# Kernel tuning notes

Hardware: AMD Instinct MI355X
Metric: run time of the kernel (lower is better)

## Reference

```python
import jax, jax.numpy as jnp
import numpy as np

MAX_WAVELENGTH = 10000.0
NUM_HEADS = 15
NUM_KV_HEADS = 5
HEAD_DIM = 64


def apply_rope(x, positions):
    """RoPE: x [B, L, H, D], positions [B, L] (int)."""
    d_half = x.shape[-1] // 2
    x = x.astype(jnp.float32)
    freq_exponents = (2.0 / x.shape[-1]) * jnp.arange(d_half, dtype=jnp.float32)
    timescale = MAX_WAVELENGTH ** freq_exponents  # [d_half]
    radians = positions[..., None].astype(jnp.float32) / timescale  # [B, L, d_half]
    radians = radians[..., None, :]  # [B, L, 1, d_half]
    sin, cos = jnp.sin(radians), jnp.cos(radians)
    x1, x2 = x[..., :d_half], x[..., d_half:]
    return jnp.concatenate([x1 * cos - x2 * sin, x2 * cos + x1 * sin], axis=-1)


def setup_inputs() -> dict:
    key = jax.random.key(0)
    k1, k2, k3, k4 = jax.random.split(key, 4)
    B, L = 2, 2048
    query_states = jax.random.normal(k1, (B, L, NUM_HEADS, HEAD_DIM), dtype=jnp.float32)
    key_states = jax.random.normal(k2, (B, L, NUM_KV_HEADS, HEAD_DIM), dtype=jnp.float32)
    value_states = jax.random.normal(k3, (B, L, NUM_KV_HEADS, HEAD_DIM), dtype=jnp.float32)
    positions = jnp.sort(jax.random.randint(k4, (B, L), 0, L, dtype=jnp.int32), axis=-1)
    # Causal (prefix-LM) boolean mask [B, L, L]
    attention_mask = jnp.broadcast_to(jnp.tril(jnp.ones((L, L), dtype=bool)), (B, L, L))
    return {
        "query_states": query_states,
        "key_states": key_states,
        "value_states": value_states,
        "positions": positions,
        "attention_mask": attention_mask,
    }


def reference(query_states, key_states, value_states, positions, attention_mask):
    B, L = query_states.shape[0], query_states.shape[1]
    groups = NUM_HEADS // NUM_KV_HEADS  # 3

    # RoPE on Q and K (eager, per original module)
    q = apply_rope(query_states, positions)  # [B, L, 15, 64] fp32
    k = apply_rope(key_states, positions)    # [B, L, 5, 64]  fp32

    # GQA expansion: [B, L, Kv, D] -> [B, L, Kv*groups, D]
    k = jnp.repeat(k, groups, axis=2)
    v = jnp.repeat(value_states, groups, axis=2).astype(jnp.float32)

    # Scores in fp32: [B, H, Lq, Lk]
    scores = jnp.einsum("bqhd,bkhd->bhqk", q, k) * (HEAD_DIM ** -0.5)
    big_neg = jnp.finfo(jnp.float32).min
    scores = jnp.where(attention_mask[:, None, :, :], scores, big_neg)
    probs = jax.nn.softmax(scores, axis=-1)

    out = jnp.einsum("bhqk,bkhd->bqhd", probs, v)  # [B, L, H, D]
    return out.reshape(B, L, NUM_HEADS * HEAD_DIM)  # [B, L, 960]
```

## Files before the change

kernel.cpp:

```cpp
#include <hip/hip_runtime.h>
#include <math.h>

#define NB 2
#define NL 2048
#define NHQ 15
#define NKV 5
#define HD 64
#define NT 32
#define GRP 3
#define PST 72
#define NWB 40
#define CST 68
#define CSLOT (32 * CST + 32)

typedef __attribute__((ext_vector_type(8))) short short8;
typedef __attribute__((ext_vector_type(4))) float floatx4;

#define ROPE_C 0.28782313662425575f
#define QSCALE 0.18033688011116016f

__device__ __forceinline__ ushort f2bf(float x) {
    unsigned u = __builtin_bit_cast(unsigned, x);
    u = (u + 0x7FFFu + ((u >> 16) & 1u)) >> 16;
    return (ushort)u;
}
__device__ __forceinline__ unsigned pk2(float a, float b) {
    unsigned ua = __builtin_bit_cast(unsigned, a) + 0x8000u;
    unsigned ub = __builtin_bit_cast(unsigned, b) + 0x8000u;
    return __builtin_amdgcn_perm(ub, ua, 0x07060302u);
}

union U8  { short8 v; ushort u[8]; };
union F8  { float4 f4[2]; float f[8]; };

__global__ __launch_bounds__(256)
void prep_kv(const float* __restrict__ K, const float* __restrict__ V,
             const int* __restrict__ pos, ushort* __restrict__ Kr,
             ushort* __restrict__ Vr) {
    __shared__ float Vs[64][65];
    const int bid = blockIdx.x, t = threadIdx.x;
    if (bid < NB * NKV * NT) {
        int b = bid / (NKV * NT), rem = bid % (NKV * NT);
        int h = rem / NT, k0 = (rem % NT) * 64;
        int j = t >> 2, c0 = t & 3;
        int row = k0 + j;
        const float* src = K + ((size_t)((b * NL + row) * NKV + h)) * HD;
        int db = c0 * 8;
        F8 x1, x2;
        x1.f4[0] = *(const float4*)&src[db];
        x1.f4[1] = *(const float4*)&src[db + 4];
        x2.f4[0] = *(const float4*)&src[db + 32];
        x2.f4[1] = *(const float4*)&src[db + 36];
        float ps = (float)pos[b * NL + row];
        U8 lo, hi;
#pragma unroll
        for (int i = 0; i < 8; ++i) {
            float inv = __expf((float)(db + i) * -ROPE_C);
            float sn, cs; __sincosf(ps * inv, &sn, &cs);
            lo.u[i] = f2bf(x1.f[i] * cs - x2.f[i] * sn);
            hi.u[i] = f2bf(x2.f[i] * cs + x1.f[i] * sn);
        }
        ushort* dst = Kr + (size_t)bid * 4096;
        *(short8*)&dst[(((j >> 4)) * 64 + c0 * 16 + (j & 15)) * 8]     = lo.v;
        *(short8*)&dst[((4 + (j >> 4)) * 64 + c0 * 16 + (j & 15)) * 8] = hi.v;
    } else {
        int vb = bid - NB * NKV * NT;
        int b = vb / (NKV * NT), rem = vb % (NKV * NT);
        int h = rem / NT, k0 = (rem % NT) * 64;
#pragma unroll
        for (int it = 0; it < 4; ++it) {
            int e = t + it * 256;
            int j = e >> 4, d4 = (e & 15) * 4;
            *(float4*)&Vs[j][d4] =
                *(const float4*)&V[((size_t)((b * NL + k0 + j) * NKV + h)) * HD + d4];
        }
        __syncthreads();
        ushort* dst = Vr + (size_t)vb * 4096;
#pragma unroll
        for (int it = 0; it < 2; ++it) {
            int o = t + it * 256;
            int d = o >> 3, c = o & 7, j0 = c * 8;
            U8 r;
#pragma unroll
            for (int k = 0; k < 8; ++k) r.u[k] = f2bf(Vs[j0 + k][d]);
            *(short8*)&dst[(((c >> 2) * 4 + (d >> 4)) * 64 + (c & 3) * 16 + (d & 15)) * 8] = r.v;
        }
    }
}

__device__ __forceinline__ void tile_step(
    int kb, bool diag, int r0, int l16, int quad, int lane,
    const ushort* Kt0, const ushort* Vt0,
    const short8 (&Qa)[2][2], floatx4 (&O)[2][4], float (&lsum)[2],
    ushort* PbW)
{
    const ushort* kt = Kt0 + (size_t)kb * 4096;
    short8 kc[8];
#pragma unroll
    for (int i = 0; i < 8; ++i)
        kc[i] = *(const short8*)&kt[((size_t)i * 64 + lane) * 8];

    floatx4 S[2][4];
#pragma unroll
    for (int rf = 0; rf < 2; ++rf)
#pragma unroll
        for (int c = 0; c < 4; ++c) S[rf][c] = (floatx4){0.f, 0.f, 0.f, 0.f};
#pragma unroll
    for (int s = 0; s < 2; ++s)
#pragma unroll
        for (int c = 0; c < 4; ++c) {
            short8 kfv = kc[s * 4 + c];
            S[0][c] = __builtin_amdgcn_mfma_f32_16x16x32_bf16(kfv, Qa[0][s], S[0][c], 0, 0, 0);
            S[1][c] = __builtin_amdgcn_mfma_f32_16x16x32_bf16(kfv, Qa[1][s], S[1][c], 0, 0, 0);
        }

    if (diag) {
#pragma unroll
        for (int rf = 0; rf < 2; ++rf) {
            int qrow = r0 + rf * 16 + l16;
            float acc = 0.f;
#pragma unroll
            for (int c = 0; c < 4; ++c) {
                float pv[4];
#pragma unroll
                for (int r = 0; r < 4; ++r) {
                    int key = kb * 64 + c * 16 + quad * 4 + r;
                    float sv = S[rf][c][r];
                    if (key > qrow) sv = -1e30f;
                    pv[r] = exp2f(sv);
                    acc += pv[r];
                }
                *(uint2*)&PbW[rf * 16 * PST + l16 * PST + c * 16 + quad * 4] =
                    make_uint2(pk2(pv[0], pv[1]), pk2(pv[2], pv[3]));
            }
            lsum[rf] += acc;
        }
    } else {
#pragma unroll
        for (int rf = 0; rf < 2; ++rf) {
            float acc = 0.f;
#pragma unroll
            for (int c = 0; c < 4; ++c) {
                float pv[4];
#pragma unroll
                for (int r = 0; r < 4; ++r) {
                    pv[r] = exp2f(S[rf][c][r]);
                    acc += pv[r];
                }
                *(uint2*)&PbW[rf * 16 * PST + l16 * PST + c * 16 + quad * 4] =
                    make_uint2(pk2(pv[0], pv[1]), pk2(pv[2], pv[3]));
            }
            lsum[rf] += acc;
        }
    }

    const ushort* vt = Vt0 + (size_t)kb * 4096;
    short8 vc[8];
#pragma unroll
    for (int i = 0; i < 8; ++i)
        vc[i] = *(const short8*)&vt[((size_t)i * 64 + lane) * 8];

#pragma unroll
    for (int s = 0; s < 2; ++s) {
        short8 pf0 = *(const short8*)&PbW[0 * 16 * PST + l16 * PST + s * 32 + quad * 8];
        short8 pf1 = *(const short8*)&PbW[1 * 16 * PST + l16 * PST + s * 32 + quad * 8];
#pragma unroll
        for (int d = 0; d < 4; ++d) {
            short8 vfv = vc[s * 4 + d];
            O[0][d] = __builtin_amdgcn_mfma_f32_16x16x32_bf16(vfv, pf0, O[0][d], 0, 0, 0);
            O[1][d] = __builtin_amdgcn_mfma_f32_16x16x32_bf16(vfv, pf1, O[1][d], 0, 0, 0);
        }
    }
}

__global__ __launch_bounds__(256, 3)
void attn_flash(const float* __restrict__ Q, const ushort* __restrict__ Kr,
                const ushort* __restrict__ Vr, const int* __restrict__ pos,
                float* __restrict__ out) {
    __shared__ __align__(16) unsigned char smem[3 * CSLOT * sizeof(float)];

    const int t = threadIdx.x;
    const int w = t >> 6, lane = t & 63;
    const int l16 = lane & 15, quad = lane >> 4;

    const int bid  = blockIdx.x;
    const int work = (bid & 7) * 150 + (bid >> 3);
    const int bh   = work / NWB;
    const int beta = work % NWB;
    const int b = bh / NHQ, h = bh % NHQ;
    const int kvh = h / GRP;

    int qi, leaderw, nch;
    if (beta < 16)      { qi = 48 + beta; leaderw = 0; nch = 4; }
    else if (beta < 32) {
        if (w < 3)      { qi = 32 + (beta - 16); leaderw = 0; nch = 3; }
        else            { qi = beta - 16;        leaderw = 3; nch = 1; }
    } else {
        int c = beta - 32;
        if (w < 2)      { qi = 16 + 2 * c; leaderw = 0; nch = 2; }
        else            { qi = 17 + 2 * c; leaderw = 2; nch = 2; }
    }
    const int ntw   = (qi >> 1) + 1;
    const int chunk = w - leaderw;
    const int kb0   = (ntw * chunk) / nch;
    const int kb1   = (ntw * (chunk + 1)) / nch;
    const int r0    = qi * 32;

    const ushort* Kt0 = Kr + (size_t)((b * NKV + kvh) * NT) * 4096;
    const ushort* Vt0 = Vr + (size_t)((b * NKV + kvh) * NT) * 4096;
    ushort* PbW = (ushort*)smem + w * 2 * 16 * PST;

    short8 Qa[2][2];
#pragma unroll
    for (int rf = 0; rf < 2; ++rf) {
        int row = r0 + rf * 16 + l16;
        const float* src = Q + ((size_t)((b * NL + row) * NHQ + h)) * HD;
        int db = quad * 8;
        F8 x1, x2;
        x1.f4[0] = *(const float4*)&src[db];
        x1.f4[1] = *(const float4*)&src[db + 4];
        x2.f4[0] = *(const float4*)&src[db + 32];
        x2.f4[1] = *(const float4*)&src[db + 36];
        float ps = (float)pos[b * NL + row];
        union { short8 v; unsigned u[4]; } lo, hi;
#pragma unroll
        for (int i = 0; i < 8; i += 2) {
            float inv0 = __expf((float)(db + i) * -ROPE_C);
            float inv1 = __expf((float)(db + i + 1) * -ROPE_C);
            float sn0, cs0, sn1, cs1;
            __sincosf(ps * inv0, &sn0, &cs0);
            __sincosf(ps * inv1, &sn1, &cs1);
            float lo0 = (x1.f[i] * cs0 - x2.f[i] * sn0) * QSCALE;
            float lo1 = (x1.f[i + 1] * cs1 - x2.f[i + 1] * sn1) * QSCALE;
            float hi0 = (x2.f[i] * cs0 + x1.f[i] * sn0) * QSCALE;
            float hi1 = (x2.f[i + 1] * cs1 + x1.f[i + 1] * sn1) * QSCALE;
            lo.u[i >> 1] = pk2(lo0, lo1);
            hi.u[i >> 1] = pk2(hi0, hi1);
        }
        Qa[rf][0] = lo.v;
        Qa[rf][1] = hi.v;
    }

    floatx4 O[2][4];
    float lsum[2] = {0.f, 0.f};
#pragma unroll
    for (int rf = 0; rf < 2; ++rf)
#pragma unroll
        for (int d = 0; d < 4; ++d) O[rf][d] = (floatx4){0.f, 0.f, 0.f, 0.f};

    for (int kb = kb0; kb < kb1; ++kb)
        tile_step(kb, kb == ntw - 1, r0, l16, quad, lane, Kt0, Vt0,
                  Qa, O, lsum, PbW);

    float ls[2];
#pragma unroll
    for (int rf = 0; rf < 2; ++rf) {
        float v = lsum[rf];
        v += __shfl_xor(v, 16, 64);
        v += __shfl_xor(v, 32, 64);
        ls[rf] = v;
    }

    __syncthreads();
    float* Cmb = (float*)smem;
    if (chunk > 0) {
        float* slot = Cmb + (size_t)(w - 1) * CSLOT;
#pragma unroll
        for (int rf = 0; rf < 2; ++rf) {
#pragma unroll
            for (int d = 0; d < 4; ++d) {
                *(float4*)&slot[(rf * 16 + l16) * CST + d * 16 + quad * 4] =
                    make_float4(O[rf][d][0], O[rf][d][1], O[rf][d][2], O[rf][d][3]);
            }
            if (quad == 0) slot[32 * CST + rf * 16 + l16] = ls[rf];
        }
    }
    __syncthreads();
    if (chunk == 0) {
        for (int m = 1; m < nch; ++m) {
            const float* slot = Cmb + (size_t)(w + m - 1) * CSLOT;
#pragma unroll
            for (int rf = 0; rf < 2; ++rf) {
#pragma unroll
                for (int d = 0; d < 4; ++d) {
                    float4 x = *(const float4*)&slot[(rf * 16 + l16) * CST + d * 16 + quad * 4];
                    O[rf][d][0] += x.x; O[rf][d][1] += x.y;
                    O[rf][d][2] += x.z; O[rf][d][3] += x.w;
                }
                ls[rf] += slot[32 * CST + rf * 16 + l16];
            }
        }
#pragma unroll
        for (int rf = 0; rf < 2; ++rf) {
            float rinv = 1.0f / ls[rf];
            int qrow = r0 + rf * 16 + l16;
            float* op = out + (size_t)(b * NL + qrow) * (NHQ * HD) + h * HD;
#pragma unroll
            for (int d = 0; d < 4; ++d) {
                float4 o = make_float4(O[rf][d][0] * rinv, O[rf][d][1] * rinv,
                                       O[rf][d][2] * rinv, O[rf][d][3] * rinv);
                *(float4*)&op[d * 16 + quad * 4] = o;
            }
        }
    }
}

extern "C" void kernel_launch(void* const* d_in, const int* in_sizes, int n_in,
                              void* d_out, int out_size, void* d_ws, size_t ws_size,
                              hipStream_t stream) {
    const float* Q   = (const float*)d_in[0];
    const float* K   = (const float*)d_in[1];
    const float* V   = (const float*)d_in[2];
    const int*   pos = (const int*)d_in[3];
    ushort* Kr = (ushort*)d_ws;
    ushort* Vr = Kr + (size_t)NB * NKV * NT * 4096;
    float*  out = (float*)d_out;

    prep_kv<<<2 * NB * NKV * NT, 256, 0, stream>>>(K, V, pos, Kr, Vr);
    attn_flash<<<NB * NHQ * NWB, 256, 0, stream>>>(Q, Kr, Vr, pos, out);
}
```

Baseline: 137.2 us.

## Keep softmax probabilities in registers and use 16x16x16 MFMA for PV

Removes the per-wave LDS staging of the probability tile by packing exp values directly into bf16 short4 operands that match the 16x16x16 MFMA B-operand layout. The V tile prep is reorganized into the matching per-lane 4-element fragment layout, and the diagonal/non-diagonal branches are merged. This eliminates LDS stores/loads and their latency inside the loop, at the cost of twice as many smaller PV MFMA instructions and more V fragment registers.

```diff
diff --git a/kernel.cpp b/kernel.cpp
--- a/kernel.cpp
+++ b/kernel.cpp
@@ -8,12 +8,12 @@
 #define HD 64
 #define NT 32
 #define GRP 3
-#define PST 72
 #define NWB 40
 #define CST 68
 #define CSLOT (32 * CST + 32)
 
 typedef __attribute__((ext_vector_type(8))) short short8;
+typedef __attribute__((ext_vector_type(4))) short short4v;
 typedef __attribute__((ext_vector_type(4))) float floatx4;
 
 #define ROPE_C 0.28782313662425575f
@@ -30,8 +30,18 @@
     return __builtin_amdgcn_perm(ub, ua, 0x07060302u);
 }
 
+__device__ __forceinline__ floatx4 mfma16(short4v a, short4v b, floatx4 c) {
+#if __has_builtin(__builtin_amdgcn_mfma_f32_16x16x16bf16_1k)
+    return __builtin_amdgcn_mfma_f32_16x16x16bf16_1k(a, b, c, 0, 0, 0);
+#else
+    asm("v_mfma_f32_16x16x16_bf16 %0, %1, %2, %0" : "+v"(c) : "v"(a), "v"(b));
+    return c;
+#endif
+}
+
 union U8  { short8 v; ushort u[8]; };
 union F8  { float4 f4[2]; float f[8]; };
+union PU  { uint2 u2; short4v v; };
 
 __global__ __launch_bounds__(256)
 void prep_kv(const float* __restrict__ K, const float* __restrict__ V,
@@ -77,13 +87,18 @@
         __syncthreads();
         ushort* dst = Vr + (size_t)vb * 4096;
 #pragma unroll
-        for (int it = 0; it < 2; ++it) {
+        for (int it = 0; it < 4; ++it) {
             int o = t + it * 256;
-            int d = o >> 3, c = o & 7, j0 = c * 8;
-            U8 r;
-#pragma unroll
-            for (int k = 0; k < 8; ++k) r.u[k] = f2bf(Vs[j0 + k][d]);
-            *(short8*)&dst[(((c >> 2) * 4 + (d >> 4)) * 64 + (c & 3) * 16 + (d & 15)) * 8] = r.v;
+            int fi = o >> 6, lane = o & 63;
+            int d = fi >> 2, c = fi & 3;
+            int l16 = lane & 15, q = lane >> 4;
+            ushort a0 = f2bf(Vs[c * 16 + q * 4 + 0][d * 16 + l16]);
+            ushort a1 = f2bf(Vs[c * 16 + q * 4 + 1][d * 16 + l16]);
+            ushort a2 = f2bf(Vs[c * 16 + q * 4 + 2][d * 16 + l16]);
+            ushort a3 = f2bf(Vs[c * 16 + q * 4 + 3][d * 16 + l16]);
+            *(uint2*)&dst[(size_t)o * 4] =
+                make_uint2((unsigned)a0 | ((unsigned)a1 << 16),
+                           (unsigned)a2 | ((unsigned)a3 << 16));
         }
     }
 }
@@ -91,8 +106,7 @@
 __device__ __forceinline__ void tile_step(
     int kb, bool diag, int r0, int l16, int quad, int lane,
     const ushort* Kt0, const ushort* Vt0,
-    const short8 (&Qa)[2][2], floatx4 (&O)[2][4], float (&lsum)[2],
-    ushort* PbW)
+    const short8 (&Qa)[2][2], floatx4 (&O)[2][4], float (&lsum)[2])
 {
     const ushort* kt = Kt0 + (size_t)kb * 4096;
     short8 kc[8];
@@ -114,61 +128,44 @@
             S[1][c] = __builtin_amdgcn_mfma_f32_16x16x32_bf16(kfv, Qa[1][s], S[1][c], 0, 0, 0);
         }
 
-    if (diag) {
-#pragma unroll
-        for (int rf = 0; rf < 2; ++rf) {
-            int qrow = r0 + rf * 16 + l16;
-            float acc = 0.f;
-#pragma unroll
-            for (int c = 0; c < 4; ++c) {
-                float pv[4];
-#pragma unroll
-                for (int r = 0; r < 4; ++r) {
+    const ushort* vt = Vt0 + (size_t)kb * 4096;
+    short4v vc[16];
+#pragma unroll
+    for (int fi = 0; fi < 16; ++fi)
+        vc[fi] = *(const short4v*)&vt[((size_t)fi * 64 + lane) * 4];
+
+    short4v P[2][4];
+#pragma unroll
+    for (int rf = 0; rf < 2; ++rf) {
+        int qrow = r0 + rf * 16 + l16;
+        float acc = 0.f;
+#pragma unroll
+        for (int c = 0; c < 4; ++c) {
+            float pv[4];
+#pragma unroll
+            for (int r = 0; r < 4; ++r) {
+                float sv = S[rf][c][r];
+                if (diag) {
                     int key = kb * 64 + c * 16 + quad * 4 + r;
-                    float sv = S[rf][c][r];
                     if (key > qrow) sv = -1e30f;
-                    pv[r] = exp2f(sv);
-                    acc += pv[r];
                 }
-                *(uint2*)&PbW[rf * 16 * PST + l16 * PST + c * 16 + quad * 4] =
-                    make_uint2(pk2(pv[0], pv[1]), pk2(pv[2], pv[3]));
+                pv[r] = exp2f(sv);
+                acc += pv[r];
             }
-            lsum[rf] += acc;
-        }
-    } else {
-#pragma unroll
-        for (int rf = 0; rf < 2; ++rf) {
-            float acc = 0.f;
-#pragma unroll
-            for (int c = 0; c < 4; ++c) {
-                float pv[4];
-#pragma unroll
-                for (int r = 0; r < 4; ++r) {
-                    pv[r] = exp2f(S[rf][c][r]);
-                    acc += pv[r];
-                }
-                *(uint2*)&PbW[rf * 16 * PST + l16 * PST + c * 16 + quad * 4] =
-                    make_uint2(pk2(pv[0], pv[1]), pk2(pv[2], pv[3]));
-            }
-            lsum[rf] += acc;
-        }
-    }
-
-    const ushort* vt = Vt0 + (size_t)kb * 4096;
-    short8 vc[8];
-#pragma unroll
-    for (int i = 0; i < 8; ++i)
-        vc[i] = *(const short8*)&vt[((size_t)i * 64 + lane) * 8];
-
-#pragma unroll
-    for (int s = 0; s < 2; ++s) {
-        short8 pf0 = *(const short8*)&PbW[0 * 16 * PST + l16 * PST + s * 32 + quad * 8];
-        short8 pf1 = *(const short8*)&PbW[1 * 16 * PST + l16 * PST + s * 32 + quad * 8];
+            PU pu;
+            pu.u2 = make_uint2(pk2(pv[0], pv[1]), pk2(pv[2], pv[3]));
+            P[rf][c] = pu.v;
+        }
+        lsum[rf] += acc;
+    }
+
+#pragma unroll
+    for (int c = 0; c < 4; ++c) {
 #pragma unroll
         for (int d = 0; d < 4; ++d) {
-            short8 vfv = vc[s * 4 + d];
-            O[0][d] = __builtin_amdgcn_mfma_f32_16x16x32_bf16(vfv, pf0, O[0][d], 0, 0, 0);
-            O[1][d] = __builtin_amdgcn_mfma_f32_16x16x32_bf16(vfv, pf1, O[1][d], 0, 0, 0);
+            short4v vf = vc[d * 4 + c];
+            O[0][d] = mfma16(vf, P[0][c], O[0][d]);
+            O[1][d] = mfma16(vf, P[1][c], O[1][d]);
         }
     }
 }
@@ -177,7 +174,7 @@
 void attn_flash(const float* __restrict__ Q, const ushort* __restrict__ Kr,
                 const ushort* __restrict__ Vr, const int* __restrict__ pos,
                 float* __restrict__ out) {
-    __shared__ __align__(16) unsigned char smem[3 * CSLOT * sizeof(float)];
+    __shared__ __align__(16) float Cmb[3 * CSLOT];
 
     const int t = threadIdx.x;
     const int w = t >> 6, lane = t & 63;
@@ -208,7 +205,6 @@
 
     const ushort* Kt0 = Kr + (size_t)((b * NKV + kvh) * NT) * 4096;
     const ushort* Vt0 = Vr + (size_t)((b * NKV + kvh) * NT) * 4096;
-    ushort* PbW = (ushort*)smem + w * 2 * 16 * PST;
 
     short8 Qa[2][2];
 #pragma unroll
@@ -250,7 +246,7 @@
 
     for (int kb = kb0; kb < kb1; ++kb)
         tile_step(kb, kb == ntw - 1, r0, l16, quad, lane, Kt0, Vt0,
-                  Qa, O, lsum, PbW);
+                  Qa, O, lsum);
 
     float ls[2];
 #pragma unroll
@@ -262,7 +258,6 @@
     }
 
     __syncthreads();
-    float* Cmb = (float*)smem;
     if (chunk > 0) {
         float* slot = Cmb + (size_t)(w - 1) * CSLOT;
 #pragma unroll
```

New measurement: 147.0 us. +7.2%, slower.

## Precompute RoPE tables in prep kernel, hoist V loads, template diagonal tile

Applied to the files above, without the earlier changes.

The K-prep kernel now writes per-position cos/sin tables to workspace, and the attention kernel reads them for Q RoPE instead of computing exp/sincos itself. The software bf16 packing is replaced with the hardware v_cvt_pk_bf16_f32 instruction. V tile loads are issued together with K loads before the QK MFMAs, and the diagonal/masked tile is split out through a template so the main loop has no mask branch. These trade extra workspace traffic and higher register pressure for less transcendental math and earlier memory latency hiding.

```diff
diff --git a/kernel.cpp b/kernel.cpp
--- a/kernel.cpp
+++ b/kernel.cpp
@@ -24,10 +24,10 @@
     u = (u + 0x7FFFu + ((u >> 16) & 1u)) >> 16;
     return (ushort)u;
 }
-__device__ __forceinline__ unsigned pk2(float a, float b) {
-    unsigned ua = __builtin_bit_cast(unsigned, a) + 0x8000u;
-    unsigned ub = __builtin_bit_cast(unsigned, b) + 0x8000u;
-    return __builtin_amdgcn_perm(ub, ua, 0x07060302u);
+__device__ __forceinline__ unsigned cvtpk(float a, float b) {
+    unsigned r;
+    asm("v_cvt_pk_bf16_f32 %0, %1, %2" : "=v"(r) : "v"(a), "v"(b));
+    return r;
 }
 
 union U8  { short8 v; ushort u[8]; };
@@ -36,7 +36,8 @@
 __global__ __launch_bounds__(256)
 void prep_kv(const float* __restrict__ K, const float* __restrict__ V,
              const int* __restrict__ pos, ushort* __restrict__ Kr,
-             ushort* __restrict__ Vr) {
+             ushort* __restrict__ Vr, float* __restrict__ Tc,
+             float* __restrict__ Ts) {
     __shared__ float Vs[64][65];
     const int bid = blockIdx.x, t = threadIdx.x;
     if (bid < NB * NKV * NT) {
@@ -52,17 +53,26 @@
         x2.f4[0] = *(const float4*)&src[db + 32];
         x2.f4[1] = *(const float4*)&src[db + 36];
         float ps = (float)pos[b * NL + row];
-        U8 lo, hi;
+        U8 lo, hi; F8 snv, csv;
 #pragma unroll
         for (int i = 0; i < 8; ++i) {
             float inv = __expf((float)(db + i) * -ROPE_C);
             float sn, cs; __sincosf(ps * inv, &sn, &cs);
+            snv.f[i] = sn; csv.f[i] = cs;
             lo.u[i] = f2bf(x1.f[i] * cs - x2.f[i] * sn);
             hi.u[i] = f2bf(x2.f[i] * cs + x1.f[i] * sn);
         }
         ushort* dst = Kr + (size_t)bid * 4096;
         *(short8*)&dst[(((j >> 4)) * 64 + c0 * 16 + (j & 15)) * 8]     = lo.v;
         *(short8*)&dst[((4 + (j >> 4)) * 64 + c0 * 16 + (j & 15)) * 8] = hi.v;
+        if (rem < NT) {
+            float* tcp = Tc + ((size_t)(b * NL + row)) * 32 + db;
+            float* tsp = Ts + ((size_t)(b * NL + row)) * 32 + db;
+            *(float4*)&tcp[0] = csv.f4[0];
+            *(float4*)&tcp[4] = csv.f4[1];
+            *(float4*)&tsp[0] = snv.f4[0];
+            *(float4*)&tsp[4] = snv.f4[1];
+        }
     } else {
         int vb = bid - NB * NKV * NT;
         int b = vb / (NKV * NT), rem = vb % (NKV * NT);
@@ -88,17 +98,22 @@
     }
 }
 
+template<bool DIAG>
 __device__ __forceinline__ void tile_step(
-    int kb, bool diag, int r0, int l16, int quad, int lane,
+    int kb, int r0, int l16, int quad, int lane,
     const ushort* Kt0, const ushort* Vt0,
     const short8 (&Qa)[2][2], floatx4 (&O)[2][4], float (&lsum)[2],
     ushort* PbW)
 {
     const ushort* kt = Kt0 + (size_t)kb * 4096;
-    short8 kc[8];
+    const ushort* vt = Vt0 + (size_t)kb * 4096;
+    short8 kc[8], vc[8];
 #pragma unroll
     for (int i = 0; i < 8; ++i)
         kc[i] = *(const short8*)&kt[((size_t)i * 64 + lane) * 8];
+#pragma unroll
+    for (int i = 0; i < 8; ++i)
+        vc[i] = *(const short8*)&vt[((size_t)i * 64 + lane) * 8];
 
     floatx4 S[2][4];
 #pragma unroll
@@ -114,51 +129,28 @@
             S[1][c] = __builtin_amdgcn_mfma_f32_16x16x32_bf16(kfv, Qa[1][s], S[1][c], 0, 0, 0);
         }
 
-    if (diag) {
-#pragma unroll
-        for (int rf = 0; rf < 2; ++rf) {
-            int qrow = r0 + rf * 16 + l16;
-            float acc = 0.f;
-#pragma unroll
-            for (int c = 0; c < 4; ++c) {
-                float pv[4];
-#pragma unroll
-                for (int r = 0; r < 4; ++r) {
+#pragma unroll
+    for (int rf = 0; rf < 2; ++rf) {
+        int qrow = r0 + rf * 16 + l16;
+        float acc = 0.f;
+#pragma unroll
+        for (int c = 0; c < 4; ++c) {
+            float pv[4];
+#pragma unroll
+            for (int r = 0; r < 4; ++r) {
+                float sv = S[rf][c][r];
+                if (DIAG) {
                     int key = kb * 64 + c * 16 + quad * 4 + r;
-                    float sv = S[rf][c][r];
                     if (key > qrow) sv = -1e30f;
-                    pv[r] = exp2f(sv);
-                    acc += pv[r];
                 }
-                *(uint2*)&PbW[rf * 16 * PST + l16 * PST + c * 16 + quad * 4] =
-                    make_uint2(pk2(pv[0], pv[1]), pk2(pv[2], pv[3]));
+                pv[r] = exp2f(sv);
+                acc += pv[r];
             }
-            lsum[rf] += acc;
-        }
-    } else {
-#pragma unroll
-        for (int rf = 0; rf < 2; ++rf) {
-            float acc = 0.f;
-#pragma unroll
-            for (int c = 0; c < 4; ++c) {
-                float pv[4];
-#pragma unroll
-                for (int r = 0; r < 4; ++r) {
-                    pv[r] = exp2f(S[rf][c][r]);
-                    acc += pv[r];
-                }
-                *(uint2*)&PbW[rf * 16 * PST + l16 * PST + c * 16 + quad * 4] =
-                    make_uint2(pk2(pv[0], pv[1]), pk2(pv[2], pv[3]));
-            }
-            lsum[rf] += acc;
-        }
-    }
-
-    const ushort* vt = Vt0 + (size_t)kb * 4096;
-    short8 vc[8];
-#pragma unroll
-    for (int i = 0; i < 8; ++i)
-        vc[i] = *(const short8*)&vt[((size_t)i * 64 + lane) * 8];
+            *(uint2*)&PbW[rf * 16 * PST + l16 * PST + c * 16 + quad * 4] =
+                make_uint2(cvtpk(pv[0], pv[1]), cvtpk(pv[2], pv[3]));
+        }
+        lsum[rf] += acc;
+    }
 
 #pragma unroll
     for (int s = 0; s < 2; ++s) {
@@ -175,8 +167,8 @@
 
 __global__ __launch_bounds__(256, 3)
 void attn_flash(const float* __restrict__ Q, const ushort* __restrict__ Kr,
-                const ushort* __restrict__ Vr, const int* __restrict__ pos,
-                float* __restrict__ out) {
+                const ushort* __restrict__ Vr, const float* __restrict__ Tc,
+                const float* __restrict__ Ts, float* __restrict__ out) {
     __shared__ __align__(16) unsigned char smem[3 * CSLOT * sizeof(float)];
 
     const int t = threadIdx.x;
@@ -216,26 +208,26 @@
         int row = r0 + rf * 16 + l16;
         const float* src = Q + ((size_t)((b * NL + row) * NHQ + h)) * HD;
         int db = quad * 8;
-        F8 x1, x2;
+        F8 x1, x2, cs8, sn8;
         x1.f4[0] = *(const float4*)&src[db];
         x1.f4[1] = *(const float4*)&src[db + 4];
         x2.f4[0] = *(const float4*)&src[db + 32];
         x2.f4[1] = *(const float4*)&src[db + 36];
-        float ps = (float)pos[b * NL + row];
+        const float* tcp = Tc + ((size_t)(b * NL + row)) * 32 + db;
+        const float* tsp = Ts + ((size_t)(b * NL + row)) * 32 + db;
+        cs8.f4[0] = *(const float4*)&tcp[0];
+        cs8.f4[1] = *(const float4*)&tcp[4];
+        sn8.f4[0] = *(const float4*)&tsp[0];
+        sn8.f4[1] = *(const float4*)&tsp[4];
         union { short8 v; unsigned u[4]; } lo, hi;
 #pragma unroll
         for (int i = 0; i < 8; i += 2) {
-            float inv0 = __expf((float)(db + i) * -ROPE_C);
-            float inv1 = __expf((float)(db + i + 1) * -ROPE_C);
-            float sn0, cs0, sn1, cs1;
-            __sincosf(ps * inv0, &sn0, &cs0);
-            __sincosf(ps * inv1, &sn1, &cs1);
-            float lo0 = (x1.f[i] * cs0 - x2.f[i] * sn0) * QSCALE;
-            float lo1 = (x1.f[i + 1] * cs1 - x2.f[i + 1] * sn1) * QSCALE;
-            float hi0 = (x2.f[i] * cs0 + x1.f[i] * sn0) * QSCALE;
-            float hi1 = (x2.f[i + 1] * cs1 + x1.f[i + 1] * sn1) * QSCALE;
-            lo.u[i >> 1] = pk2(lo0, lo1);
-            hi.u[i >> 1] = pk2(hi0, hi1);
+            float lo0 = (x1.f[i] * cs8.f[i] - x2.f[i] * sn8.f[i]) * QSCALE;
+            float lo1 = (x1.f[i + 1] * cs8.f[i + 1] - x2.f[i + 1] * sn8.f[i + 1]) * QSCALE;
+            float hi0 = (x2.f[i] * cs8.f[i] + x1.f[i] * sn8.f[i]) * QSCALE;
+            float hi1 = (x2.f[i + 1] * cs8.f[i + 1] + x1.f[i + 1] * sn8.f[i + 1]) * QSCALE;
+            lo.u[i >> 1] = cvtpk(lo0, lo1);
+            hi.u[i >> 1] = cvtpk(hi0, hi1);
         }
         Qa[rf][0] = lo.v;
         Qa[rf][1] = hi.v;
@@ -248,9 +240,11 @@
 #pragma unroll
         for (int d = 0; d < 4; ++d) O[rf][d] = (floatx4){0.f, 0.f, 0.f, 0.f};
 
-    for (int kb = kb0; kb < kb1; ++kb)
-        tile_step(kb, kb == ntw - 1, r0, l16, quad, lane, Kt0, Vt0,
-                  Qa, O, lsum, PbW);
+    const int kbe = (kb1 == ntw) ? ntw - 1 : kb1;
+    for (int kb = kb0; kb < kbe; ++kb)
+        tile_step<false>(kb, r0, l16, quad, lane, Kt0, Vt0, Qa, O, lsum, PbW);
+    if (kb1 == ntw)
+        tile_step<true>(ntw - 1, r0, l16, quad, lane, Kt0, Vt0, Qa, O, lsum, PbW);
 
     float ls[2];
 #pragma unroll
@@ -314,8 +308,10 @@
     const int*   pos = (const int*)d_in[3];
     ushort* Kr = (ushort*)d_ws;
     ushort* Vr = Kr + (size_t)NB * NKV * NT * 4096;
+    float*  Tc = (float*)(Vr + (size_t)NB * NKV * NT * 4096);
+    float*  Ts = Tc + (size_t)NB * NL * 32;
     float*  out = (float*)d_out;
 
-    prep_kv<<<2 * NB * NKV * NT, 256, 0, stream>>>(K, V, pos, Kr, Vr);
-    attn_flash<<<NB * NHQ * NWB, 256, 0, stream>>>(Q, Kr, Vr, pos, out);
-}
+    prep_kv<<<2 * NB * NKV * NT, 256, 0, stream>>>(K, V, pos, Kr, Vr, Tc, Ts);
+    attn_flash<<<NB * NHQ * NWB, 256, 0, stream>>>(Q, Kr, Vr, Tc, Ts, out);
+}
```

Measured after the change: 141.0 us. +2.8%, slower.
